# Kernel optimization log

Hardware: AMD Instinct MI355X
Metric: run time of the kernel (lower is better)

Reference implementation:

```python
import jax, jax.numpy as jnp
import numpy as np

KERNEL_SIZE = 3


def extract_local_features(feature_map, point_coords, kernel_size=KERNEL_SIZE):
    # feature_map: (B,C,H,W); point_coords: (B,N,2) normalized (y,x) in [0,1]
    B, C, H, W = feature_map.shape
    half = kernel_size // 2
    x = (point_coords[..., 1] * (W - 1)).astype(jnp.int32)  # (B,N)
    y = (point_coords[..., 0] * (H - 1)).astype(jnp.int32)
    x_min = jnp.clip(x - half, 0, None)
    x_max = jnp.clip(x + half + 1, None, W)
    y_min = jnp.clip(y - half, 0, None)
    y_max = jnpp_clip = jnp.clip(y + half + 1, None, H)
    y_max = jnp.clip(y + half + 1, None, H)
    # gather a fixed (k,k) window with clamped offsets, mask out-of-window entries
    offs = jnp.arange(kernel_size)  # (k,)
    yy = y_min[..., None] + offs  # (B,N,k) candidate rows
    xx = x_min[..., None] + offs  # (B,N,k)
    y_valid = yy < y_max[..., None]
    x_valid = xx < x_max[..., None]
    yy_c = jnp.clip(yy, 0, H - 1)
    xx_c = jnp.clip(xx, 0, W - 1)
    # flat spatial indices (B,N,k,k)
    flat_idx = yy_c[..., :, None] * W + xx_c[..., None, :]
    valid = (y_valid[..., :, None] & x_valid[..., None, :]).astype(feature_map.dtype)
    fm_flat = feature_map.reshape(B, C, H * W)  # (B,C,HW)

    def per_batch(fm, idx, val):
        # fm: (C,HW); idx,val: (N,k,k)
        g = fm[:, idx.reshape(-1)].reshape(fm.shape[0], *idx.shape)  # (C,N,k,k)
        s = jnp.einsum('cnij,nij->cn', g, val)
        cnt = val.sum(axis=(-1, -2))  # (N,)
        return s / cnt[None, :]

    return jax.vmap(per_batch)(fm_flat, flat_idx, valid)  # (B,C,N)


def point_sample(inp, point_coords):
    # bilinear grid_sample, align_corners=False, coords in [0,1] as (x,y) order
    # per the code: grid = 2*coords - 1; grid_sample uses (x,y) convention
    B, C, H, W = inp.shape
    gx = point_coords[..., 0]  # (B,N) in [0,1]
    gy = point_coords[..., 1]
    # align_corners=False mapping: pix = ((g*2-1)+1)/2 * size - 0.5 = g*size - 0.5
    fx = gx * W - 0.5
    fy = gy * H - 0.5
    x0 = jnp.floor(fx).astype(jnp.int32)
    y0 = jnp.floor(fy).astype(jnp.int32)
    wx = fx - x0
    wy = fy - y0

    def gather(yc, xc):
        inb = ((yc >= 0) & (yc < H) & (xc >= 0) & (xc < W)).astype(inp.dtype)  # (B,N)
        ycc = jnp.clip(yc, 0, H - 1)
        xcc = jnp.clip(xc, 0, W - 1)
        flat = ycc * W + xcc  # (B,N)
        fm = inp.reshape(B, C, H * W)
        g = jax.vmap(lambda f, i: f[:, i])(fm, flat)  # (B,C,N)
        return g * inb[:, None, :]

    v00 = gather(y0, x0)
    v01 = gather(y0, x0 + 1)
    v10 = gather(y0 + 1, x0)
    v11 = gather(y0 + 1, x0 + 1)
    wx_ = wx[:, None, :]
    wy_ = wy[:, None, :]
    out = (v00 * (1 - wx_) * (1 - wy_) + v01 * wx_ * (1 - wy_)
           + v10 * (1 - wx_) * wy_ + v11 * wx_ * wy_)  # (B,C,N)
    return out.transpose(0, 2, 1)  # (B,N,C)


def calculate_uncertainty(mask_logits):
    return -jnp.abs(mask_logits).squeeze(1)  # (B,H,W)


def edge_topk_sampling(edge_masks, uncertainty_map, topk):
    # edge_masks: (B,H,W) {0,1}; uncertainty_map: (B,H,W)
    B, H, W = edge_masks.shape
    NEG = jnp.asarray(-1e30, uncertainty_map.dtype)
    masked_u = jnp.where(edge_masks.reshape(B, -1) == 1,
                         uncertainty_map.reshape(B, -1), NEG)
    vals, idx = jax.lax.top_k(masked_u, topk)  # (B,topk)
    yi = (idx // W).astype(jnp.float32)
    xi = (idx % W).astype(jnp.float32)
    coords = jnp.stack([yi / (H - 1), xi / (W - 1)], axis=-1)  # (B,topk,2) (y,x)
    return idx, coords


def setup_inputs() -> dict:
    key = jax.random.key(0)
    k1, k2, k3, k4 = jax.random.split(key, 4)
    B, C, H, W = 8, 256, 256, 256
    N = 4096
    feature_map = jax.random.normal(k1, (B, C, H, W), dtype=jnp.float32)
    pred_mask = jax.random.normal(k2, (B, 1, H, W), dtype=jnp.float32)
    edge_masks = jax.random.randint(k3, (B, H, W), 0, 2).astype(jnp.int32)
    point_coords = jax.random.uniform(k4, (B, N, 2), dtype=jnp.float32)
    return {"feature_map": feature_map, "pred_mask": pred_mask,
            "edge_masks": edge_masks, "point_coords": point_coords,
            "topk": 4096}


def reference(feature_map, pred_mask, edge_masks, point_coords, topk):
    uncertainty_map = calculate_uncertainty(pred_mask)  # (B,H,W)
    idx, important_coords = edge_topk_sampling(edge_masks, uncertainty_map, topk)
    local_feats = extract_local_features(feature_map, important_coords)  # (B,C,topk)
    sampled = point_sample(feature_map, point_coords)  # (B,N,C)
    return local_feats, sampled, important_coords, idx
```

## Files before the change

kernel.cpp:

```cpp
#include <hip/hip_runtime.h>

#define CC 256
#define HH 256
#define WW 256
#define HWV 65536
#define NN 4096
#define SROWS 18
#define SSTRIDE 260

using u64 = unsigned long long;
using u32 = unsigned int;

__device__ __forceinline__ u32 lbound(const u32* __restrict__ a, u32 n, u32 key) {
    u32 lo = 0, hi = n;
    while (lo < hi) { u32 mid = (lo + hi) >> 1; if (a[mid] < key) lo = mid + 1; else hi = mid; }
    return lo;
}

__global__ void zero_hist_k(u32* __restrict__ ghist) {
    ghist[blockIdx.x * 1024 + threadIdx.x] = 0u;
}

__global__ __launch_bounds__(256) void build_keys_hist_k(const float* __restrict__ pm,
                                                         const int* __restrict__ em,
                                                         u64* __restrict__ keys,
                                                         u32* __restrict__ ghist) {
    __shared__ u32 h[4096];
    const int t = threadIdx.x;
    #pragma unroll
    for (int q = 0; q < 16; ++q) h[t + q * 256] = 0u;
    __syncthreads();
    int i = blockIdx.x * 256 + t;
    int b = i >> 16;
    float f = (em[i] == 1) ? -fabsf(pm[i]) : -1e30f;
    u32 u = __float_as_uint(f);
    u32 k = (u & 0x80000000u) ? ~u : (u | 0x80000000u);
    u64 K = ((u64)k << 16) | (u64)(0xFFFFu - ((u32)i & 0xFFFFu));
    keys[i] = K;
    atomicAdd(&h[(u32)(K >> 36)], 1u);
    __syncthreads();
    u32* gh = ghist + b * 4096;
    #pragma unroll
    for (int q = 0; q < 16; ++q) {
        u32 v = h[t + q * 256];
        if (v) atomicAdd(&gh[t + q * 256], v);
    }
}

__global__ __launch_bounds__(1024) void topk_sortpc_k(const u64* __restrict__ keys,
                                                      const u32* __restrict__ ghist,
                                                      const float* __restrict__ pc,
                                                      u32* __restrict__ pixSorted,
                                                      u32* __restrict__ pcSorted,
                                                      float* __restrict__ outCoord,
                                                      float* __restrict__ outIdx) {
    __shared__ u64 sel[NN];
    __shared__ u64 bm[1024];
    __shared__ u32 wp[1024];
    __shared__ u32 s_digit, s_rem, s_cnt;
    const int t = threadIdx.x;
    if (blockIdx.x < 8) {
        const int b = blockIdx.x;
        const u64* kb = keys + (size_t)b * HWV;
        u32* hist = (u32*)sel;
        u64 prefix = 0ULL;
        u32 remaining = NN;
        for (int r = 0; r < 4; ++r) {
            int shift = 36 - 12 * r;
            if (r == 0) {
                #pragma unroll
                for (int q = 0; q < 4; ++q) hist[t + q * 1024] = ghist[b * 4096 + t + q * 1024];
                __syncthreads();
            } else {
                #pragma unroll
                for (int q = 0; q < 4; ++q) hist[t + q * 1024] = 0u;
                __syncthreads();
                for (int i = t; i < HWV; i += 1024) {
                    u64 K = kb[i];
                    if ((K >> (shift + 12)) == prefix)
                        atomicAdd(&hist[(u32)((K >> shift) & 0xFFFULL)], 1u);
                }
                __syncthreads();
            }
            for (int off = 1; off < 4096; off <<= 1) {
                u32 v[4];
                #pragma unroll
                for (int q = 0; q < 4; ++q) {
                    int i = t + q * 1024;
                    v[q] = hist[i];
                    if (i + off < 4096) v[q] += hist[i + off];
                }
                __syncthreads();
                #pragma unroll
                for (int q = 0; q < 4; ++q) hist[t + q * 1024] = v[q];
                __syncthreads();
            }
            #pragma unroll
            for (int q = 0; q < 4; ++q) {
                int d = t + q * 1024;
                u32 ge = hist[d];
                u32 gt = (d < 4095) ? hist[d + 1] : 0u;
                if (ge >= remaining && gt < remaining) { s_digit = (u32)d; s_rem = remaining - gt; }
            }
            __syncthreads();
            prefix = (prefix << 12) | (u64)s_digit;
            remaining = s_rem;
            __syncthreads();
        }
        if (t == 0) s_cnt = 0u;
        __syncthreads();
        for (int i = t; i < HWV; i += 1024) {
            u64 K = kb[i];
            if (K >= prefix) { u32 p = atomicAdd(&s_cnt, 1u); sel[p] = K; }
        }
        __syncthreads();
        for (int k = 2; k <= NN; k <<= 1) {
            for (int j = k >> 1; j > 0; j >>= 1) {
                for (int i = t; i < NN; i += 1024) {
                    int l = i ^ j;
                    if (l > i) {
                        u64 a = sel[i], c = sel[l];
                        bool asc = ((i & k) == 0);
                        if ((a < c) == asc) { sel[i] = c; sel[l] = a; }
                    }
                }
                __syncthreads();
            }
        }
        bm[t] = 0ULL;
        __syncthreads();
        #pragma unroll
        for (int q = 0; q < 4; ++q) {
            int r = t + q * 1024;
            u32 pix = 0xFFFFu - (u32)(sel[r] & 0xFFFFULL);
            u32 yi = pix >> 8, xi = pix & 255u;
            outCoord[((size_t)b * NN + r) * 2 + 0] = (float)yi / 255.0f;
            outCoord[((size_t)b * NN + r) * 2 + 1] = (float)xi / 255.0f;
            outIdx[b * NN + r] = (float)pix;
            atomicOr(&bm[pix >> 6], 1ULL << (pix & 63));
        }
        __syncthreads();
        wp[t] = (u32)__popcll(bm[t]);
        __syncthreads();
        for (int off = 1; off < 1024; off <<= 1) {
            u32 v = wp[t];
            if (t >= off) v += wp[t - off];
            __syncthreads();
            wp[t] = v;
            __syncthreads();
        }
        #pragma unroll
        for (int q = 0; q < 4; ++q) {
            int r = t + q * 1024;
            u32 pix = 0xFFFFu - (u32)(sel[r] & 0xFFFFULL);
            int w = (int)(pix >> 6);
            u32 pos = wp[w] - (u32)__popcll(bm[w])
                    + (u32)__popcll(bm[w] & ((1ULL << (pix & 63)) - 1ULL));
            pixSorted[b * NN + pos] = (pix << 12) | (u32)r;
        }
    } else {
        const int b = blockIdx.x - 8;
        u32* cellArr = (u32*)sel;
        u32* hist256 = wp;
        u32* cnt     = (u32*)bm;
        if (t < 256) { hist256[t] = 0u; cnt[t] = 0u; }
        __syncthreads();
        for (int n = t; n < NN; n += 1024) {
            float gx = pc[((size_t)b * NN + n) * 2 + 0];
            float gy = pc[((size_t)b * NN + n) * 2 + 1];
            float fx = gx * 256.0f - 0.5f;
            float fy = gy * 256.0f - 0.5f;
            int x0 = (int)floorf(fx), y0 = (int)floorf(fy);
            int xc = min(max(x0, 0), 255), yc = min(max(y0, 0), 255);
            cellArr[n] = ((u32)(yc * 256 + xc) << 12) | (u32)n;
            atomicAdd(&hist256[yc], 1u);
        }
        __syncthreads();
        for (int off = 1; off < 256; off <<= 1) {
            u32 v = 0;
            if (t < 256) { v = hist256[t]; if (t >= off) v += hist256[t - off]; }
            __syncthreads();
            if (t < 256) hist256[t] = v;
            __syncthreads();
        }
        for (int n = t; n < NN; n += 1024) {
            u32 pk = cellArr[n];
            u32 yc = pk >> 20;
            u32 base = (yc > 0) ? hist256[yc - 1] : 0u;
            u32 pos = base + atomicAdd(&cnt[yc], 1u);
            pcSorted[b * NN + pos] = pk;
        }
    }
}

#define STAGE_LOAD(plane) \
    { int idx, r, c4, gr; \
      idx = t;        r = idx >> 6; c4 = idx & 63; gr = min(max(rStart + r, 0), HH - 1); \
      g0 = *(const float4*)((plane) + gr * WW + c4 * 4); \
      idx = t + 256;  r = idx >> 6; c4 = idx & 63; gr = min(max(rStart + r, 0), HH - 1); \
      g1 = *(const float4*)((plane) + gr * WW + c4 * 4); \
      idx = t + 512;  r = idx >> 6; c4 = idx & 63; gr = min(max(rStart + r, 0), HH - 1); \
      g2 = *(const float4*)((plane) + gr * WW + c4 * 4); \
      idx = t + 768;  r = idx >> 6; c4 = idx & 63; gr = min(max(rStart + r, 0), HH - 1); \
      g3 = *(const float4*)((plane) + gr * WW + c4 * 4); \
      if (t < 128) { idx = t + 1024; r = idx >> 6; c4 = idx & 63; gr = min(max(rStart + r, 0), HH - 1); \
      g4 = *(const float4*)((plane) + gr * WW + c4 * 4); } }

#define STAGE_WRITE() \
    { int idx, r, c4; \
      idx = t;        r = idx >> 6; c4 = idx & 63; *(float4*)(sm + r * SSTRIDE + c4 * 4) = g0; \
      idx = t + 256;  r = idx >> 6; c4 = idx & 63; *(float4*)(sm + r * SSTRIDE + c4 * 4) = g1; \
      idx = t + 512;  r = idx >> 6; c4 = idx & 63; *(float4*)(sm + r * SSTRIDE + c4 * 4) = g2; \
      idx = t + 768;  r = idx >> 6; c4 = idx & 63; *(float4*)(sm + r * SSTRIDE + c4 * 4) = g3; \
      if (t < 128) { idx = t + 1024; r = idx >> 6; c4 = idx & 63; *(float4*)(sm + r * SSTRIDE + c4 * 4) = g4; } }

__global__ __launch_bounds__(256) void plane_gather_k(const float* __restrict__ fm,
                                                      const float* __restrict__ pc,
                                                      const u32* __restrict__ pixSorted,
                                                      const u32* __restrict__ pcSorted,
                                                      float* __restrict__ outLc,
                                                      float* __restrict__ outSc) {
    __shared__ float sm[SROWS * SSTRIDE];
    const int band = blockIdx.x, c0 = blockIdx.y * 32, b = blockIdx.z;
    const int t = threadIdx.x;
    const int rStart = band * 16 - 1;
    const u32 keyLo = (u32)band << 24, keyHi = (u32)(band + 1) << 24;
    const u32* aL = pixSorted + b * NN;
    const u32* aS = pcSorted + b * NN;
    u32 loL = lbound(aL, NN, keyLo), cL = lbound(aL, NN, keyHi) - loL;
    u32 loS = lbound(aS, NN, keyLo), cS = lbound(aS, NN, keyHi) - loS;
    const float* planes = fm + ((size_t)b * CC + c0) * HWV;
    const float* pcb = pc + (size_t)b * NN * 2;

    int  Lo0 = 0, Lr2 = 0;  float Lw0 = 0, Lw1 = 0, Lw2 = 0, Lw3 = 0, Lwr = 0, Lic = 0;
    int  Mo0 = 0, Mr2 = 0;  float Mw0 = 0, Mw1 = 0, Mw2 = 0, Mw3 = 0, Mwr = 0, Mic = 0;
    int  So0 = 0, Sr1 = 0;  float Sv0 = 0, Sv1 = 0, Sw0 = 0, Sw1 = 0;
    int  To0 = 0, Tr1 = 0;  float Tv0 = 0, Tv1 = 0, Tw0 = 0, Tw1 = 0;
    {
        u32 jl = (u32)t;
        if (jl < cL) {
            u32 pix = aL[loL + jl] >> 12;
            int yi = (int)(pix >> 8), xi = (int)(pix & 255u);
            float cy = (float)yi / 255.0f, cx = (float)xi / 255.0f;
            int x = (int)(cx * 255.0f), y = (int)(cy * 255.0f);
            int x_min = max(x - 1, 0), x_max = min(x + 2, WW);
            int y_min = max(y - 1, 0), hgt = min(y + 2, HH) - y_min;
            int base2 = min(x_min & ~1, WW - 4);
            Lw0 = (base2 + 0 >= x_min && base2 + 0 < x_max) ? 1.0f : 0.0f;
            Lw1 = (base2 + 1 >= x_min && base2 + 1 < x_max) ? 1.0f : 0.0f;
            Lw2 = (base2 + 2 >= x_min && base2 + 2 < x_max) ? 1.0f : 0.0f;
            Lw3 = (base2 + 3 >= x_min && base2 + 3 < x_max) ? 1.0f : 0.0f;
            Lo0 = (y_min - rStart) * SSTRIDE + base2;
            Lr2 = ((hgt == 3) ? 2 : 0) * SSTRIDE;  Lwr = (hgt == 3) ? 1.0f : 0.0f;
            Lic = 1.0f / (float)((x_max - x_min) * hgt);
        }
        jl = 256u + (u32)t;
        if (jl < cL) {
            u32 pix = aL[loL + jl] >> 12;
            int yi = (int)(pix >> 8), xi = (int)(pix & 255u);
            float cy = (float)yi / 255.0f, cx = (float)xi / 255.0f;
            int x = (int)(cx * 255.0f), y = (int)(cy * 255.0f);
            int x_min = max(x - 1, 0), x_max = min(x + 2, WW);
            int y_min = max(y - 1, 0), hgt = min(y + 2, HH) - y_min;
            int base2 = min(x_min & ~1, WW - 4);
            Mw0 = (base2 + 0 >= x_min && base2 + 0 < x_max) ? 1.0f : 0.0f;
            Mw1 = (base2 + 1 >= x_min && base2 + 1 < x_max) ? 1.0f : 0.0f;
            Mw2 = (base2 + 2 >= x_min && base2 + 2 < x_max) ? 1.0f : 0.0f;
            Mw3 = (base2 + 3 >= x_min && base2 + 3 < x_max) ? 1.0f : 0.0f;
            Mo0 = (y_min - rStart) * SSTRIDE + base2;
            Mr2 = ((hgt == 3) ? 2 : 0) * SSTRIDE;  Mwr = (hgt == 3) ? 1.0f : 0.0f;
            Mic = 1.0f / (float)((x_max - x_min) * hgt);
        }
        u32 js = (u32)t;
        if (js < cS) {
            u32 sn = aS[loS + js] & 0xFFFu;
            float gx = pcb[2 * sn + 0], gy = pcb[2 * sn + 1];
            float fx = gx * 256.0f - 0.5f, fy = gy * 256.0f - 0.5f;
            float fx0 = floorf(fx), fy0 = floorf(fy);
            int x0 = (int)fx0, y0 = (int)fy0;
            float wx = fx - fx0, wy = fy - fy0;
            int xb = min(max(x0, 0), WW - 2);
            if (x0 < 0)            { Sv0 = wx;        Sv1 = 0.0f; }
            else if (x0 >= WW - 1) { Sv0 = 0.0f;      Sv1 = 1.0f - wx; }
            else                   { Sv0 = 1.0f - wx; Sv1 = wx; }
            Sw0 = (y0 >= 0)     ? (1.0f - wy) : 0.0f;
            Sw1 = (y0 + 1 < HH) ? wy          : 0.0f;
            int yc0 = min(max(y0, 0), HH - 1), yc1 = min(max(y0 + 1, 0), HH - 1);
            So0 = (yc0 - rStart) * SSTRIDE + xb;
            Sr1 = (yc1 - yc0) * SSTRIDE;
        }
        js = 256u + (u32)t;
        if (js < cS) {
            u32 sn = aS[loS + js] & 0xFFFu;
            float gx = pcb[2 * sn + 0], gy = pcb[2 * sn + 1];
            float fx = gx * 256.0f - 0.5f, fy = gy * 256.0f - 0.5f;
            float fx0 = floorf(fx), fy0 = floorf(fy);
            int x0 = (int)fx0, y0 = (int)fy0;
            float wx = fx - fx0, wy = fy - fy0;
            int xb = min(max(x0, 0), WW - 2);
            if (x0 < 0)            { Tv0 = wx;        Tv1 = 0.0f; }
            else if (x0 >= WW - 1) { Tv0 = 0.0f;      Tv1 = 1.0f - wx; }
            else                   { Tv0 = 1.0f - wx; Tv1 = wx; }
            Tw0 = (y0 >= 0)     ? (1.0f - wy) : 0.0f;
            Tw1 = (y0 + 1 < HH) ? wy          : 0.0f;
            int yc0 = min(max(y0, 0), HH - 1), yc1 = min(max(y0 + 1, 0), HH - 1);
            To0 = (yc0 - rStart) * SSTRIDE + xb;
            Tr1 = (yc1 - yc0) * SSTRIDE;
        }
    }

    float4 g0, g1, g2, g3, g4;
    STAGE_LOAD(planes)
    STAGE_WRITE()
    __syncthreads();

    #pragma unroll 1
    for (int j = 0; j < 32; ++j) {
        if (j + 1 < 32) { const float* np = planes + (size_t)(j + 1) * HWV; STAGE_LOAD(np) }
        float* oL = outLc + ((size_t)(b * CC + c0 + j)) * NN + loL;
        float* oS = outSc + ((size_t)(b * CC + c0 + j)) * NN + loS;
        if ((u32)t < cL) {
            float2 a0 = *(const float2*)(sm + Lo0);
            float2 b0 = *(const float2*)(sm + Lo0 + 2);
            float2 a1 = *(const float2*)(sm + Lo0 + SSTRIDE);
            float2 b1 = *(const float2*)(sm + Lo0 + SSTRIDE + 2);
            float2 a2 = *(const float2*)(sm + Lo0 + Lr2);
            float2 b2 = *(const float2*)(sm + Lo0 + Lr2 + 2);
            float r0 = a0.x * Lw0 + a0.y * Lw1 + b0.x * Lw2 + b0.y * Lw3;
            float r1 = a1.x * Lw0 + a1.y * Lw1 + b1.x * Lw2 + b1.y * Lw3;
            float r2 = a2.x * Lw0 + a2.y * Lw1 + b2.x * Lw2 + b2.y * Lw3;
            oL[t] = (r0 + r1 + Lwr * r2) * Lic;
        }
        if (256u + (u32)t < cL) {
            float2 a0 = *(const float2*)(sm + Mo0);
            float2 b0 = *(const float2*)(sm + Mo0 + 2);
            float2 a1 = *(const float2*)(sm + Mo0 + SSTRIDE);
            float2 b1 = *(const float2*)(sm + Mo0 + SSTRIDE + 2);
            float2 a2 = *(const float2*)(sm + Mo0 + Mr2);
            float2 b2 = *(const float2*)(sm + Mo0 + Mr2 + 2);
            float r0 = a0.x * Mw0 + a0.y * Mw1 + b0.x * Mw2 + b0.y * Mw3;
            float r1 = a1.x * Mw0 + a1.y * Mw1 + b1.x * Mw2 + b1.y * Mw3;
            float r2 = a2.x * Mw0 + a2.y * Mw1 + b2.x * Mw2 + b2.y * Mw3;
            oL[256 + t] = (r0 + r1 + Mwr * r2) * Mic;
        }
        if ((u32)t < cS) {
            oS[t] = Sw0 * (sm[So0] * Sv0 + sm[So0 + 1] * Sv1)
                  + Sw1 * (sm[So0 + Sr1] * Sv0 + sm[So0 + Sr1 + 1] * Sv1);
        }
        if (256u + (u32)t < cS) {
            oS[256 + t] = Tw0 * (sm[To0] * Tv0 + sm[To0 + 1] * Tv1)
                        + Tw1 * (sm[To0 + Tr1] * Tv0 + sm[To0 + Tr1 + 1] * Tv1);
        }
        __syncthreads();
        if (j + 1 < 32) { STAGE_WRITE() }
        __syncthreads();
    }

    for (u32 jl = 512 + (u32)t; jl < cL; jl += 256) {
        u32 pix = aL[loL + jl] >> 12;
        int yi = (int)(pix >> 8), xi = (int)(pix & 255u);
        float cy = (float)yi / 255.0f, cx = (float)xi / 255.0f;
        int x = (int)(cx * 255.0f), y = (int)(cy * 255.0f);
        int x_min = max(x - 1, 0), x_max = min(x + 2, WW);
        int y_min = max(y - 1, 0), y_max = min(y + 2, HH);
        float ic = 1.0f / (float)((x_max - x_min) * (y_max - y_min));
        for (int j = 0; j < 32; ++j) {
            const float* p = planes + (size_t)j * HWV;
            float s = 0.0f;
            for (int yy = y_min; yy < y_max; ++yy)
                for (int xx = x_min; xx < x_max; ++xx) s += p[yy * WW + xx];
            outLc[((size_t)(b * CC + c0 + j)) * NN + loL + jl] = s * ic;
        }
    }
    for (u32 js = 512 + (u32)t; js < cS; js += 256) {
        u32 sn = aS[loS + js] & 0xFFFu;
        float gx = pcb[2 * sn + 0], gy = pcb[2 * sn + 1];
        float fx = gx * 256.0f - 0.5f, fy = gy * 256.0f - 0.5f;
        float fx0 = floorf(fx), fy0 = floorf(fy);
        int x0 = (int)fx0, y0 = (int)fy0;
        float wx = fx - fx0, wy = fy - fy0;
        int xb = min(max(x0, 0), WW - 2);
        float v0, v1, r0, r1;
        if (x0 < 0)            { v0 = wx;        v1 = 0.0f; }
        else if (x0 >= WW - 1) { v0 = 0.0f;      v1 = 1.0f - wx; }
        else                   { v0 = 1.0f - wx; v1 = wx; }
        r0 = (y0 >= 0)     ? (1.0f - wy) : 0.0f;
        r1 = (y0 + 1 < HH) ? wy          : 0.0f;
        int yc0 = min(max(y0, 0), HH - 1), yc1 = min(max(y0 + 1, 0), HH - 1);
        int o0 = yc0 * WW + xb, o1 = yc1 * WW + xb;
        for (int j = 0; j < 32; ++j) {
            const float* p = planes + (size_t)j * HWV;
            outSc[((size_t)(b * CC + c0 + j)) * NN + loS + js] =
                r0 * (p[o0] * v0 + p[o0 + 1] * v1) + r1 * (p[o1] * v0 + p[o1 + 1] * v1);
        }
    }
}

__global__ __launch_bounds__(256) void unpermL_k(const float* __restrict__ outLc,
                                                 const u32* __restrict__ pixSorted,
                                                 float* __restrict__ outL) {
    __shared__ float row[NN];
    const int c = blockIdx.x, b = blockIdx.y;
    const int t = threadIdx.x;
    const float* in = outLc + ((size_t)(b * CC + c)) * NN;
    for (int j = t; j < NN; j += 256)
        row[pixSorted[b * NN + j] & 0xFFFu] = in[j];
    __syncthreads();
    float* o = outL + ((size_t)(b * CC + c)) * NN;
    for (int i = t; i < NN; i += 256) o[i] = row[i];
}

__global__ __launch_bounds__(256) void unpermS_k(const float* __restrict__ outSc,
                                                 const u32* __restrict__ pcSorted,
                                                 float* __restrict__ outS) {
    __shared__ float tile[32][257];
    __shared__ u32 ns[256];
    const int j0 = blockIdx.x * 256, c0 = blockIdx.y * 32, b = blockIdx.z;
    const int t = threadIdx.x;
    ns[t] = pcSorted[b * NN + j0 + t] & 0xFFFu;
    for (int i = 0; i < 32; ++i)
        tile[i][t] = outSc[((size_t)(b * CC + c0 + i)) * NN + j0 + t];
    __syncthreads();
    for (int idx = t; idx < 8192; idx += 256) {
        int p = idx >> 5, k = idx & 31;
        outS[((size_t)b * NN + ns[p]) * CC + c0 + k] = tile[k][p];
    }
}

__global__ void build_keys_k(const float* __restrict__ pm, const int* __restrict__ em,
                             u64* __restrict__ keys) {
    int i = blockIdx.x * blockDim.x + threadIdx.x;
    float f = (em[i] == 1) ? -fabsf(pm[i]) : -1e30f;
    u32 u = __float_as_uint(f);
    u32 k = (u & 0x80000000u) ? ~u : (u | 0x80000000u);
    u32 pix = (u32)i & 0xFFFFu;
    keys[i] = ((u64)k << 16) | (u64)(0xFFFFu - pix);
}

__global__ __launch_bounds__(1024) void topk_sortpc_old_k(const u64* __restrict__ keys,
                                                          const float* __restrict__ pc,
                                                          u32* __restrict__ stash,
                                                          u32* __restrict__ pixSorted,
                                                          u32* __restrict__ pcSorted) {
    __shared__ u64 sel[NN];
    __shared__ u64 bm[1024];
    __shared__ u32 wp[1024];
    __shared__ u32 s_digit, s_rem, s_cnt;
    const int t = threadIdx.x;
    if (blockIdx.x < 8) {
        const int b = blockIdx.x;
        const u64* kb = keys + (size_t)b * HWV;
        u32* hist = (u32*)sel;
        u64 prefix = 0ULL;
        u32 remaining = NN;
        for (int r = 0; r < 4; ++r) {
            int shift = 36 - 12 * r;
            #pragma unroll
            for (int q = 0; q < 4; ++q) hist[t + q * 1024] = 0u;
            __syncthreads();
            for (int i = t; i < HWV; i += 1024) {
                u64 K = kb[i];
                if ((K >> (shift + 12)) == prefix)
                    atomicAdd(&hist[(u32)((K >> shift) & 0xFFFULL)], 1u);
            }
            __syncthreads();
            for (int off = 1; off < 4096; off <<= 1) {
                u32 v[4];
                #pragma unroll
                for (int q = 0; q < 4; ++q) {
                    int i = t + q * 1024;
                    v[q] = hist[i];
                    if (i + off < 4096) v[q] += hist[i + off];
                }
                __syncthreads();
                #pragma unroll
                for (int q = 0; q < 4; ++q) hist[t + q * 1024] = v[q];
                __syncthreads();
            }
            #pragma unroll
            for (int q = 0; q < 4; ++q) {
                int d = t + q * 1024;
                u32 ge = hist[d];
                u32 gt = (d < 4095) ? hist[d + 1] : 0u;
                if (ge >= remaining && gt < remaining) { s_digit = (u32)d; s_rem = remaining - gt; }
            }
            __syncthreads();
            prefix = (prefix << 12) | (u64)s_digit;
            remaining = s_rem;
            __syncthreads();
        }
        if (t == 0) s_cnt = 0u;
        __syncthreads();
        for (int i = t; i < HWV; i += 1024) {
            u64 K = kb[i];
            if (K >= prefix) { u32 p = atomicAdd(&s_cnt, 1u); sel[p] = K; }
        }
        __syncthreads();
        for (int k = 2; k <= NN; k <<= 1) {
            for (int j = k >> 1; j > 0; j >>= 1) {
                for (int i = t; i < NN; i += 1024) {
                    int l = i ^ j;
                    if (l > i) {
                        u64 a = sel[i], c = sel[l];
                        bool asc = ((i & k) == 0);
                        if ((a < c) == asc) { sel[i] = c; sel[l] = a; }
                    }
                }
                __syncthreads();
            }
        }
        bm[t] = 0ULL;
        __syncthreads();
        #pragma unroll
        for (int q = 0; q < 4; ++q) {
            int r = t + q * 1024;
            u32 pix = 0xFFFFu - (u32)(sel[r] & 0xFFFFULL);
            stash[b * NN + r] = pix;
            atomicOr(&bm[pix >> 6], 1ULL << (pix & 63));
        }
        __syncthreads();
        wp[t] = (u32)__popcll(bm[t]);
        __syncthreads();
        for (int off = 1; off < 1024; off <<= 1) {
            u32 v = wp[t];
            if (t >= off) v += wp[t - off];
            __syncthreads();
            wp[t] = v;
            __syncthreads();
        }
        #pragma unroll
        for (int q = 0; q < 4; ++q) {
            int r = t + q * 1024;
            u32 pix = 0xFFFFu - (u32)(sel[r] & 0xFFFFULL);
            int w = (int)(pix >> 6);
            u32 pos = wp[w] - (u32)__popcll(bm[w])
                    + (u32)__popcll(bm[w] & ((1ULL << (pix & 63)) - 1ULL));
            pixSorted[b * NN + pos] = (pix << 12) | (u32)r;
        }
    } else {
        const int b = blockIdx.x - 8;
        u32* cellArr = (u32*)sel;
        u32* hist256 = wp;
        u32* cnt     = (u32*)bm;
        if (t < 256) { hist256[t] = 0u; cnt[t] = 0u; }
        __syncthreads();
        for (int n = t; n < NN; n += 1024) {
            float gx = pc[((size_t)b * NN + n) * 2 + 0];
            float gy = pc[((size_t)b * NN + n) * 2 + 1];
            float fx = gx * 256.0f - 0.5f;
            float fy = gy * 256.0f - 0.5f;
            int x0 = (int)floorf(fx), y0 = (int)floorf(fy);
            int xc = min(max(x0, 0), 255), yc = min(max(y0, 0), 255);
            cellArr[n] = ((u32)(yc * 256 + xc) << 12) | (u32)n;
            atomicAdd(&hist256[yc], 1u);
        }
        __syncthreads();
        for (int off = 1; off < 256; off <<= 1) {
            u32 v = 0;
            if (t < 256) { v = hist256[t]; if (t >= off) v += hist256[t - off]; }
            __syncthreads();
            if (t < 256) hist256[t] = v;
            __syncthreads();
        }
        for (int n = t; n < NN; n += 1024) {
            u32 pk = cellArr[n];
            u32 yc = pk >> 20;
            u32 base = (yc > 0) ? hist256[yc - 1] : 0u;
            u32 pos = base + atomicAdd(&cnt[yc], 1u);
            pcSorted[b * NN + pos] = pk;
        }
    }
}

template<int MODE>
__global__ __launch_bounds__(256, 4) void gather_k(const float* __restrict__ fm,
                                                   const float* __restrict__ pc,
                                                   const u32* __restrict__ pixSorted,
                                                   const u32* __restrict__ pcSorted,
                                                   float* __restrict__ outLp,
                                                   float* __restrict__ outS) {
    __shared__ float tile[256][33];
    __shared__ u32 pidx[256];
    const int b = blockIdx.z, j0 = blockIdx.x * 256, t = threadIdx.x;
    bool doL = (MODE == 1); int c0 = blockIdx.y * 32;
    const float* planes = fm + ((size_t)b * CC + c0) * HWV;
    if (doL) {
        u32 packed = pixSorted[b * NN + j0 + t];
        u32 pix = packed >> 12;
        pidx[t] = packed & 0xFFFu;
        int yi = (int)(pix >> 8), xi = (int)(pix & 255u);
        float cy = (float)yi / 255.0f, cx = (float)xi / 255.0f;
        int x = (int)(cx * 255.0f), y = (int)(cy * 255.0f);
        int x_min = max(x - 1, 0), x_max = min(x + 2, WW);
        int y_min = max(y - 1, 0), y_max = min(y + 2, HH);
        int base = min(x_min & ~3, WW - 8);
        float w8[8];
        #pragma unroll
        for (int i = 0; i < 8; ++i)
            w8[i] = (base + i >= x_min && base + i < x_max) ? 1.0f : 0.0f;
        float wr2 = (y_min + 2 < y_max) ? 1.0f : 0.0f;
        int o0 = y_min * WW + base, o1 = o0 + WW;
        int o2 = min(y_min + 2, HH - 1) * WW + base;
        float invc = 1.0f / (float)((x_max - x_min) * (y_max - y_min));
        #pragma unroll 2
        for (int j = 0; j < 32; ++j) {
            const float* p = planes + (size_t)j * HWV;
            float4 a0 = *(const float4*)(p + o0), b0 = *(const float4*)(p + o0 + 4);
            float4 a1 = *(const float4*)(p + o1), b1 = *(const float4*)(p + o1 + 4);
            float4 a2 = *(const float4*)(p + o2), b2 = *(const float4*)(p + o2 + 4);
            float s0 = a0.x * w8[0] + a0.y * w8[1] + a0.z * w8[2] + a0.w * w8[3]
                     + b0.x * w8[4] + b0.y * w8[5] + b0.z * w8[6] + b0.w * w8[7];
            float s1 = a1.x * w8[0] + a1.y * w8[1] + a1.z * w8[2] + a1.w * w8[3]
                     + b1.x * w8[4] + b1.y * w8[5] + b1.z * w8[6] + b1.w * w8[7];
            float s2 = a2.x * w8[0] + a2.y * w8[1] + a2.z * w8[2] + a2.w * w8[3]
                     + b2.x * w8[4] + b2.y * w8[5] + b2.z * w8[6] + b2.w * w8[7];
            tile[t][j] = (s0 + s1 + wr2 * s2) * invc;
        }
        __syncthreads();
        for (int idx = t; idx < 8192; idx += 256) {
            int p = idx >> 5, k = idx & 31;
            outLp[((size_t)b * NN + pidx[p]) * CC + c0 + k] = tile[p][k];
        }
    } else {
        int n = (int)(pcSorted[b * NN + j0 + t] & 0xFFFu);
        pidx[t] = (u32)n;
        float gx = pc[((size_t)b * NN + n) * 2 + 0];
        float gy = pc[((size_t)b * NN + n) * 2 + 1];
        float fx = gx * 256.0f - 0.5f, fy = gy * 256.0f - 0.5f;
        float fx0 = floorf(fx), fy0 = floorf(fy);
        int x0 = (int)fx0, y0 = (int)fy0;
        float wx = fx - fx0, wy = fy - fy0;
        int xb = min(max(x0, 0), WW - 2);
        float wv0, wv1;
        if (x0 < 0)            { wv0 = wx;        wv1 = 0.0f; }
        else if (x0 >= WW - 1) { wv0 = 0.0f;      wv1 = 1.0f - wx; }
        else                   { wv0 = 1.0f - wx; wv1 = wx; }
        float wr0 = (y0 >= 0)     ? (1.0f - wy) : 0.0f;
        float wr1 = (y0 + 1 < HH) ? wy          : 0.0f;
        int yc0 = min(max(y0, 0), HH - 1), yc1 = min(max(y0 + 1, 0), HH - 1);
        int o0 = yc0 * WW + xb, o1 = yc1 * WW + xb;
        #pragma unroll 4
        for (int j = 0; j < 32; ++j) {
            const float* p = planes + (size_t)j * HWV;
            tile[t][j] = wr0 * (p[o0] * wv0 + p[o0 + 1] * wv1)
                       + wr1 * (p[o1] * wv0 + p[o1 + 1] * wv1);
        }
        __syncthreads();
        for (int idx = t; idx < 8192; idx += 256) {
            int p = idx >> 5, k = idx & 31;
            outS[((size_t)b * NN + pidx[p]) * CC + c0 + k] = tile[p][k];
        }
    }
}

__global__ __launch_bounds__(256) void transpose_k(const float* __restrict__ outLp,
                                                   float* __restrict__ outL) {
    __shared__ float tile[256][33];
    const int b = blockIdx.z, c0 = blockIdx.y * 32, r0 = blockIdx.x * 256;
    const int t = threadIdx.x;
    for (int idx = t; idx < 8192; idx += 256) {
        int p = idx >> 5, k = idx & 31;
        tile[p][k] = outLp[((size_t)b * NN + r0 + p) * CC + c0 + k];
    }
    __syncthreads();
    for (int idx = t; idx < 8192; idx += 256) {
        int cl = idx >> 8, col = idx & 255;
        outL[((size_t)b * CC + c0 + cl) * NN + r0 + col] = tile[col][cl];
    }
}

__global__ void emit_k(const u32* __restrict__ stash, float* __restrict__ outCoord,
                       float* __restrict__ outIdx) {
    int i = blockIdx.x * blockDim.x + threadIdx.x;
    u32 p = stash[i];
    u32 yi = p >> 8, xi = p & 255u;
    outCoord[(size_t)i * 2 + 0] = (float)yi / 255.0f;
    outCoord[(size_t)i * 2 + 1] = (float)xi / 255.0f;
    outIdx[i] = (float)p;
}

extern "C" void kernel_launch(void* const* d_in, const int* in_sizes, int n_in,
                              void* d_out, int out_size, void* d_ws, size_t ws_size,
                              hipStream_t stream) {
    const float* fm = (const float*)d_in[0];
    const float* pm = (const float*)d_in[1];
    const int*   em = (const int*)d_in[2];
    const float* pc = (const float*)d_in[3];
    (void)in_sizes; (void)n_in; (void)out_size;

    float* out      = (float*)d_out;
    float* outL     = out;
    float* outS     = out + (size_t)8388608;
    float* outCoord = out + (size_t)16777216;
    float* outIdx   = out + (size_t)16842752;

    const size_t need_ws = (size_t)80 * 1024 * 1024;
    bool ws_ok = ws_size >= need_ws;

    if (ws_ok) {
        char* w = (char*)d_ws;
        u64* keys      = (u64*)w;
        u32* ghist     = (u32*)(w + (size_t)4096 * 1024);
        u32* pixSorted = (u32*)(w + (size_t)4300 * 1024);
        u32* pcSorted  = (u32*)(w + (size_t)4600 * 1024);
        float* outLc   = (float*)(w + (size_t)5  * 1024 * 1024);
        float* outSc   = (float*)(w + (size_t)40 * 1024 * 1024);

        hipLaunchKernelGGL(zero_hist_k, dim3(32), dim3(1024), 0, stream, ghist);
        hipLaunchKernelGGL(build_keys_hist_k, dim3(2048), dim3(256), 0, stream,
                           pm, em, keys, ghist);
        hipLaunchKernelGGL(topk_sortpc_k, dim3(16), dim3(1024), 0, stream,
                           keys, ghist, pc, pixSorted, pcSorted, outCoord, outIdx);
        hipLaunchKernelGGL(plane_gather_k, dim3(16, 8, 8), dim3(256), 0, stream,
                           fm, pc, pixSorted, pcSorted, outLc, outSc);
        hipLaunchKernelGGL(unpermL_k, dim3(256, 8), dim3(256), 0, stream,
                           outLc, pixSorted, outL);
        hipLaunchKernelGGL(unpermS_k, dim3(16, 8, 8), dim3(256), 0, stream,
                           outSc, pcSorted, outS);
    } else {
        u64* keys      = (u64*)outS;
        u32* stash     = (u32*)outIdx;
        u32* pixSorted = (u32*)outCoord;
        u32* pcSorted  = pixSorted + 32768;
        float* outLp   = outS;

        hipLaunchKernelGGL(build_keys_k, dim3(2048), dim3(256), 0, stream, pm, em, keys);
        hipLaunchKernelGGL(topk_sortpc_old_k, dim3(16), dim3(1024), 0, stream,
                           keys, pc, stash, pixSorted, pcSorted);
        hipLaunchKernelGGL((gather_k<1>), dim3(16, 8, 8), dim3(256), 0, stream,
                           fm, pc, pixSorted, pcSorted, outLp, outS);
        hipLaunchKernelGGL(transpose_k, dim3(16, 8, 8), dim3(256), 0, stream, outLp, outL);
        hipLaunchKernelGGL((gather_k<2>), dim3(16, 8, 8), dim3(256), 0, stream,
                           fm, pc, pixSorted, pcSorted, outS, outS);
        hipLaunchKernelGGL(emit_k, dim3(128), dim3(256), 0, stream, stash, outCoord, outIdx);
    }
}
```

Baseline: 311.2 us.

## Shortcut radix select with bitonic sort of top bucket; double-buffer gather staging

The top-k radix select now checks after the first 12-bit digit whether the boundary bucket holds at most NN keys. If it does, it collects that bucket into shared memory, bitonic-sorts it and reads the threshold directly, skipping the three further histogram passes over all 65536 keys. The plane gather kernel also gets two shared staging buffers, so the next plane can be written without waiting on a barrier, which drops one __syncthreads per channel iteration at the cost of doubled LDS use.

```diff
diff --git a/kernel.cpp b/kernel.cpp
--- a/kernel.cpp
+++ b/kernel.cpp
@@ -57,21 +57,69 @@
     __shared__ u64 sel[NN];
     __shared__ u64 bm[1024];
     __shared__ u32 wp[1024];
-    __shared__ u32 s_digit, s_rem, s_cnt;
+    __shared__ u32 s_digit, s_rem, s_cnt, s_C;
     const int t = threadIdx.x;
     if (blockIdx.x < 8) {
         const int b = blockIdx.x;
         const u64* kb = keys + (size_t)b * HWV;
         u32* hist = (u32*)sel;
-        u64 prefix = 0ULL;
-        u32 remaining = NN;
-        for (int r = 0; r < 4; ++r) {
-            int shift = 36 - 12 * r;
-            if (r == 0) {
-                #pragma unroll
-                for (int q = 0; q < 4; ++q) hist[t + q * 1024] = ghist[b * 4096 + t + q * 1024];
-                __syncthreads();
-            } else {
+        #pragma unroll
+        for (int q = 0; q < 4; ++q) hist[t + q * 1024] = ghist[b * 4096 + t + q * 1024];
+        __syncthreads();
+        for (int off = 1; off < 4096; off <<= 1) {
+            u32 v[4];
+            #pragma unroll
+            for (int q = 0; q < 4; ++q) {
+                int i = t + q * 1024;
+                v[q] = hist[i];
+                if (i + off < 4096) v[q] += hist[i + off];
+            }
+            __syncthreads();
+            #pragma unroll
+            for (int q = 0; q < 4; ++q) hist[t + q * 1024] = v[q];
+            __syncthreads();
+        }
+        #pragma unroll
+        for (int q = 0; q < 4; ++q) {
+            int d = t + q * 1024;
+            u32 ge = hist[d];
+            u32 gt = (d < 4095) ? hist[d + 1] : 0u;
+            if (ge >= NN && gt < NN) { s_digit = (u32)d; s_rem = NN - gt; s_C = ge - gt; }
+        }
+        __syncthreads();
+        const u32 dig = s_digit, rem = s_rem, C = s_C;
+        u64 prefix;
+        __syncthreads();
+        if (C <= (u32)NN) {
+            if (t == 0) s_cnt = 0u;
+            #pragma unroll
+            for (int q = 0; q < 4; ++q) sel[t + q * 1024] = 0ULL;
+            __syncthreads();
+            for (int i = t; i < HWV; i += 1024) {
+                u64 K = kb[i];
+                if ((u32)(K >> 36) == dig) { u32 p = atomicAdd(&s_cnt, 1u); sel[p] = K; }
+            }
+            __syncthreads();
+            for (int k = 2; k <= NN; k <<= 1) {
+                for (int j = k >> 1; j > 0; j >>= 1) {
+                    for (int i = t; i < NN; i += 1024) {
+                        int l = i ^ j;
+                        if (l > i) {
+                            u64 a = sel[i], c = sel[l];
+                            bool asc = ((i & k) == 0);
+                            if ((a < c) == asc) { sel[i] = c; sel[l] = a; }
+                        }
+                    }
+                    __syncthreads();
+                }
+            }
+            prefix = sel[rem - 1];
+            __syncthreads();
+        } else {
+            prefix = (u64)dig;
+            u32 remaining = rem;
+            for (int r = 1; r < 4; ++r) {
+                int shift = 36 - 12 * r;
                 #pragma unroll
                 for (int q = 0; q < 4; ++q) hist[t + q * 1024] = 0u;
                 __syncthreads();
@@ -81,31 +129,31 @@
                         atomicAdd(&hist[(u32)((K >> shift) & 0xFFFULL)], 1u);
                 }
                 __syncthreads();
-            }
-            for (int off = 1; off < 4096; off <<= 1) {
-                u32 v[4];
+                for (int off = 1; off < 4096; off <<= 1) {
+                    u32 v[4];
+                    #pragma unroll
+                    for (int q = 0; q < 4; ++q) {
+                        int i = t + q * 1024;
+                        v[q] = hist[i];
+                        if (i + off < 4096) v[q] += hist[i + off];
+                    }
+                    __syncthreads();
+                    #pragma unroll
+                    for (int q = 0; q < 4; ++q) hist[t + q * 1024] = v[q];
+                    __syncthreads();
+                }
                 #pragma unroll
                 for (int q = 0; q < 4; ++q) {
-                    int i = t + q * 1024;
-                    v[q] = hist[i];
-                    if (i + off < 4096) v[q] += hist[i + off];
+                    int d = t + q * 1024;
+                    u32 ge = hist[d];
+                    u32 gt = (d < 4095) ? hist[d + 1] : 0u;
+                    if (ge >= remaining && gt < remaining) { s_digit = (u32)d; s_rem = remaining - gt; }
                 }
                 __syncthreads();
-                #pragma unroll
-                for (int q = 0; q < 4; ++q) hist[t + q * 1024] = v[q];
+                prefix = (prefix << 12) | (u64)s_digit;
+                remaining = s_rem;
                 __syncthreads();
             }
-            #pragma unroll
-            for (int q = 0; q < 4; ++q) {
-                int d = t + q * 1024;
-                u32 ge = hist[d];
-                u32 gt = (d < 4095) ? hist[d + 1] : 0u;
-                if (ge >= remaining && gt < remaining) { s_digit = (u32)d; s_rem = remaining - gt; }
-            }
-            __syncthreads();
-            prefix = (prefix << 12) | (u64)s_digit;
-            remaining = s_rem;
-            __syncthreads();
         }
         if (t == 0) s_cnt = 0u;
         __syncthreads();
@@ -206,13 +254,13 @@
       if (t < 128) { idx = t + 1024; r = idx >> 6; c4 = idx & 63; gr = min(max(rStart + r, 0), HH - 1); \
       g4 = *(const float4*)((plane) + gr * WW + c4 * 4); } }
 
-#define STAGE_WRITE() \
+#define STAGE_WRITE(dst) \
     { int idx, r, c4; \
-      idx = t;        r = idx >> 6; c4 = idx & 63; *(float4*)(sm + r * SSTRIDE + c4 * 4) = g0; \
-      idx = t + 256;  r = idx >> 6; c4 = idx & 63; *(float4*)(sm + r * SSTRIDE + c4 * 4) = g1; \
-      idx = t + 512;  r = idx >> 6; c4 = idx & 63; *(float4*)(sm + r * SSTRIDE + c4 * 4) = g2; \
-      idx = t + 768;  r = idx >> 6; c4 = idx & 63; *(float4*)(sm + r * SSTRIDE + c4 * 4) = g3; \
-      if (t < 128) { idx = t + 1024; r = idx >> 6; c4 = idx & 63; *(float4*)(sm + r * SSTRIDE + c4 * 4) = g4; } }
+      idx = t;        r = idx >> 6; c4 = idx & 63; *(float4*)((dst) + r * SSTRIDE + c4 * 4) = g0; \
+      idx = t + 256;  r = idx >> 6; c4 = idx & 63; *(float4*)((dst) + r * SSTRIDE + c4 * 4) = g1; \
+      idx = t + 512;  r = idx >> 6; c4 = idx & 63; *(float4*)((dst) + r * SSTRIDE + c4 * 4) = g2; \
+      idx = t + 768;  r = idx >> 6; c4 = idx & 63; *(float4*)((dst) + r * SSTRIDE + c4 * 4) = g3; \
+      if (t < 128) { idx = t + 1024; r = idx >> 6; c4 = idx & 63; *(float4*)((dst) + r * SSTRIDE + c4 * 4) = g4; } }
 
 __global__ __launch_bounds__(256) void plane_gather_k(const float* __restrict__ fm,
                                                       const float* __restrict__ pc,
@@ -220,7 +268,8 @@
                                                       const u32* __restrict__ pcSorted,
                                                       float* __restrict__ outLc,
                                                       float* __restrict__ outSc) {
-    __shared__ float sm[SROWS * SSTRIDE];
+    __shared__ float smA[SROWS * SSTRIDE];
+    __shared__ float smB[SROWS * SSTRIDE];
     const int band = blockIdx.x, c0 = blockIdx.y * 32, b = blockIdx.z;
     const int t = threadIdx.x;
     const int rStart = band * 16 - 1;
@@ -311,11 +360,13 @@
 
     float4 g0, g1, g2, g3, g4;
     STAGE_LOAD(planes)
-    STAGE_WRITE()
+    STAGE_WRITE(smA)
     __syncthreads();
 
     #pragma unroll 1
     for (int j = 0; j < 32; ++j) {
+        const float* sm = (j & 1) ? smB : smA;
+        float* smw = (j & 1) ? smA : smB;
         if (j + 1 < 32) { const float* np = planes + (size_t)(j + 1) * HWV; STAGE_LOAD(np) }
         float* oL = outLc + ((size_t)(b * CC + c0 + j)) * NN + loL;
         float* oS = outSc + ((size_t)(b * CC + c0 + j)) * NN + loS;
@@ -351,8 +402,7 @@
             oS[256 + t] = Tw0 * (sm[To0] * Tv0 + sm[To0 + 1] * Tv1)
                         + Tw1 * (sm[To0 + Tr1] * Tv0 + sm[To0 + Tr1 + 1] * Tv1);
         }
-        __syncthreads();
-        if (j + 1 < 32) { STAGE_WRITE() }
+        if (j + 1 < 32) { STAGE_WRITE(smw) }
         __syncthreads();
     }
 
```

Result: slower. 331.2 us (+6.4%).
